# Optimization experiments

Hardware: AMD Instinct MI355X
Metric: run time of the kernel (lower is better)

The kernel has to match this reference:

```python
import jax, jax.numpy as jnp
import numpy as np

DIM = 256
NUM_HEADS = 8
HEAD_DIM = DIM // NUM_HEADS          # 32
KEY_DIM = int(HEAD_DIM * 0.5)        # 16
SCALE = KEY_DIM ** (-0.5)
QKV_OUT = DIM + 2 * KEY_DIM * NUM_HEADS  # 512
BN_EPS = 1e-3


def _bn(x, gamma, beta, mean, var):
    # inference-mode BatchNorm2d over channel axis 1 of NCHW
    inv = gamma / jnp.sqrt(var + BN_EPS)
    return x * inv[None, :, None, None] + (beta - mean * inv)[None, :, None, None]


def _conv1x1(x, w):
    # w: (O, C, 1, 1)
    return jnp.einsum('bchw,oc->bohw', x, w[:, :, 0, 0])


def _dwconv3x3(x, w):
    # depthwise 3x3, SAME padding; w: (C, 1, 3, 3)
    return jax.lax.conv_general_dilated(
        x, w, window_strides=(1, 1), padding='SAME',
        feature_group_count=x.shape[1],
        dimension_numbers=('NCHW', 'OIHW', 'NCHW'))


def setup_inputs() -> dict:
    key = jax.random.key(0)
    ks = jax.random.split(key, 16)
    B, C, H, W = 16, DIM, 32, 32
    inp = {
        'x': jax.random.normal(ks[0], (B, C, H, W), jnp.float32),
        'qkv_w': jax.random.normal(ks[1], (QKV_OUT, DIM, 1, 1), jnp.float32) * (1.0 / np.sqrt(DIM)),
        'qkv_gamma': jnp.ones((QKV_OUT,), jnp.float32),
        'qkv_beta': jnp.zeros((QKV_OUT,), jnp.float32),
        'qkv_mean': jax.random.normal(ks[2], (QKV_OUT,), jnp.float32) * 0.1,
        'qkv_var': jax.random.uniform(ks[3], (QKV_OUT,), jnp.float32, 0.5, 1.5),
        'pe_w': jax.random.normal(ks[4], (DIM, 1, 3, 3), jnp.float32) * (1.0 / 3.0),
        'pe_gamma': jnp.ones((DIM,), jnp.float32),
        'pe_beta': jnp.zeros((DIM,), jnp.float32),
        'pe_mean': jax.random.normal(ks[5], (DIM,), jnp.float32) * 0.1,
        'pe_var': jax.random.uniform(ks[6], (DIM,), jnp.float32, 0.5, 1.5),
        'proj_w': jax.random.normal(ks[7], (DIM, DIM, 1, 1), jnp.float32) * (1.0 / np.sqrt(DIM)),
        'proj_gamma': jnp.ones((DIM,), jnp.float32),
        'proj_beta': jnp.zeros((DIM,), jnp.float32),
        'proj_mean': jax.random.normal(ks[8], (DIM,), jnp.float32) * 0.1,
        'proj_var': jax.random.uniform(ks[9], (DIM,), jnp.float32, 0.5, 1.5),
    }
    return inp


def reference(x, qkv_w, qkv_gamma, qkv_beta, qkv_mean, qkv_var,
              pe_w, pe_gamma, pe_beta, pe_mean, pe_var,
              proj_w, proj_gamma, proj_beta, proj_mean, proj_var):
    B, C, H, W = x.shape
    N = H * W
    # qkv: 1x1 conv + BN (act=False)
    qkv = _bn(_conv1x1(x, qkv_w), qkv_gamma, qkv_beta, qkv_mean, qkv_var)
    qkv = qkv.reshape(B, NUM_HEADS, 2 * KEY_DIM + HEAD_DIM, N)
    q = qkv[:, :, :KEY_DIM]                          # (B, h, kd, N)
    k = qkv[:, :, KEY_DIM:2 * KEY_DIM]               # (B, h, kd, N)
    v = qkv[:, :, 2 * KEY_DIM:]                      # (B, h, hd, N)
    # attn = (q^T @ k) * scale, softmax over last dim
    attn = jnp.einsum('bhdn,bhdm->bhnm', q, k) * SCALE   # (B, h, N, N)
    attn = jax.nn.softmax(attn, axis=-1)
    # v @ attn^T
    v_attn = jnp.einsum('bhdn,bhmn->bhdm', v, attn)      # (B, h, hd, N)
    v_attn = v_attn.reshape(B, C, H, W)
    v_reshaped = v.reshape(B, C, H, W)
    pos_enc = _bn(_dwconv3x3(v_reshaped, pe_w), pe_gamma, pe_beta, pe_mean, pe_var)
    out = v_attn + pos_enc
    out = _bn(_conv1x1(out, proj_w), proj_gamma, proj_beta, proj_mean, proj_var)
    return out
```

## Files before the change

### kernel.cpp

```cpp
#include <hip/hip_runtime.h>

#define B_ 16
#define C_ 256
#define N_ 1024
#define NH 8
#define HD 32
#define KD 16
#define QKV_OUT_ 512
#define BN_EPS 1e-3f
#define SCALE2_ (0.25f * 1.44269504088896f)

typedef __attribute__((ext_vector_type(8))) short short8;
typedef __attribute__((ext_vector_type(16))) float float16;

__device__ inline unsigned short f2bf(float f) {
  unsigned int u = __float_as_uint(f);
  return (unsigned short)((u + 0x7FFF + ((u >> 16) & 1)) >> 16);
}
__device__ inline float bf2f(unsigned short s) {
  return __uint_as_float(((unsigned int)s) << 16);
}
__device__ inline float16 zero16() {
  float16 z;
  #pragma unroll
  for (int i = 0; i < 16; ++i) z[i] = 0.f;
  return z;
}
__device__ inline unsigned int pack_bf16_trunc(float a, float b) {
  return __builtin_amdgcn_perm(__float_as_uint(b), __float_as_uint(a), 0x07060302u);
}
__device__ inline unsigned int pack_bf16_rne(float a, float b) {
  return (unsigned int)f2bf(a) | ((unsigned int)f2bf(b) << 16);
}
__device__ inline float fast_exp2(float x) {
#if __has_builtin(__builtin_amdgcn_exp2f)
  return __builtin_amdgcn_exp2f(x);
#else
  return exp2f(x);
#endif
}
__device__ inline void pl32(unsigned int& a, unsigned int& b) {
#if __has_builtin(__builtin_amdgcn_permlane32_swap)
  typedef __attribute__((ext_vector_type(2))) int int2v;
  int2v r = __builtin_amdgcn_permlane32_swap((int)a, (int)b, false, false);
  a = (unsigned int)r[0];
  b = (unsigned int)r[1];
#else
  unsigned int ea = (unsigned int)__shfl_xor((int)a, 32, 64);
  unsigned int eb = (unsigned int)__shfl_xor((int)b, 32, 64);
  bool hi = (threadIdx.x & 32) != 0;
  unsigned int an = hi ? eb : a;
  unsigned int bn = hi ? b : ea;
  a = an; b = bn;
#endif
}
__device__ inline short8 lds_frag(const unsigned short* p) {
  union { uint2 u[2]; short8 s; } r;
  r.u[0] = *(const uint2*)p;
  r.u[1] = *(const uint2*)(p + 4);
  return r.s;
}
__device__ inline void lds_store16(unsigned short* p, uint4 v) {
  *(uint2*)p = make_uint2(v.x, v.y);
  *(uint2*)(p + 4) = make_uint2(v.z, v.w);
}

__global__ __launch_bounds__(256) void fold_weights(
    const float* __restrict__ qkv_w, const float* __restrict__ qg,
    const float* __restrict__ qb, const float* __restrict__ qm,
    const float* __restrict__ qv,
    const float* __restrict__ proj_w, const float* __restrict__ pg,
    const float* __restrict__ pb, const float* __restrict__ pm,
    const float* __restrict__ pv,
    unsigned short* __restrict__ wq, float* __restrict__ biasq,
    unsigned short* __restrict__ wp, float* __restrict__ biasp)
{
  const int o = blockIdx.x, c = threadIdx.x;
  if (o < QKV_OUT_) {
    float s = ((o & 63) < 16) ? SCALE2_ : 1.f;
    float inv = qg[o] * rsqrtf(qv[o] + BN_EPS) * s;
    wq[o * C_ + c] = f2bf(qkv_w[o * C_ + c] * inv);
    if (c == 0) biasq[o] = qb[o] * s - qm[o] * inv;
  } else {
    int oo = o - QKV_OUT_;
    float inv = pg[oo] * rsqrtf(pv[oo] + BN_EPS);
    wp[oo * C_ + c] = f2bf(proj_w[oo * C_ + c] * inv);
    if (c == 0) biasp[oo] = pb[oo] - pm[oo] * inv;
  }
}

__global__ __launch_bounds__(256) void gemm_qkv(
    const float* __restrict__ x, const unsigned short* __restrict__ wq,
    const float* __restrict__ bias,
    unsigned short* __restrict__ qkT, unsigned short* __restrict__ vbuf)
{
  constexpr int STR = 44;
  __shared__ __align__(8) unsigned short wa[2][128 * STR];
  __shared__ __align__(8) unsigned short xb[2][128 * STR];
  const int tid = threadIdx.x;
  const int wave = tid >> 6, lane = tid & 63, l31 = lane & 31, lh = lane >> 5;
  const int wm = wave & 1, wn = wave >> 1;
  const int b = blockIdx.x >> 3, nloc = (blockIdx.x & 7) * 128;
  const int o0 = blockIdx.y * 128;

  const int r0 = tid >> 2, oc0 = (tid & 3) * 8;
  const int r1 = r0 + 64;
  const int tok = tid & 127, chalf = (tid >> 7) * 16;
  const float* xbase = x + (size_t)b * C_ * N_ + nloc + tok;

  uint4 ga0, ga1;
  float nb[16];

  auto loadk = [&](int kc) {
    ga0 = *(const uint4*)(wq + (size_t)(o0 + r0) * C_ + kc * 32 + oc0);
    ga1 = *(const uint4*)(wq + (size_t)(o0 + r1) * C_ + kc * 32 + oc0);
    #pragma unroll
    for (int j = 0; j < 16; ++j)
      nb[j] = xbase[(size_t)(kc * 32 + chalf + j) * N_];
  };
  auto storek = [&](int bufi) {
    lds_store16(&wa[bufi][r0 * STR + oc0], ga0);
    lds_store16(&wa[bufi][r1 * STR + oc0], ga1);
    unsigned int pk[8];
    #pragma unroll
    for (int q = 0; q < 8; ++q) pk[q] = pack_bf16_rne(nb[2 * q], nb[2 * q + 1]);
    lds_store16(&xb[bufi][tok * STR + chalf], make_uint4(pk[0], pk[1], pk[2], pk[3]));
    lds_store16(&xb[bufi][tok * STR + chalf + 8], make_uint4(pk[4], pk[5], pk[6], pk[7]));
  };

  float16 acc[2][2];
  #pragma unroll
  for (int i = 0; i < 2; ++i)
    #pragma unroll
    for (int j = 0; j < 2; ++j) acc[i][j] = zero16();

  loadk(0);
  storek(0);
  __syncthreads();

  for (int kc = 0; kc < 8; ++kc) {
    const int buf = kc & 1;
    if (kc < 7) loadk(kc + 1);

    #pragma unroll
    for (int ks = 0; ks < 2; ++ks) {
      const int ko = ks * 16 + lh * 8;
      short8 a0 = lds_frag(&wa[buf][(wm * 64 + l31) * STR + ko]);
      short8 a1 = lds_frag(&wa[buf][(wm * 64 + 32 + l31) * STR + ko]);
      short8 b0 = lds_frag(&xb[buf][(wn * 64 + l31) * STR + ko]);
      short8 b1 = lds_frag(&xb[buf][(wn * 64 + 32 + l31) * STR + ko]);
      acc[0][0] = __builtin_amdgcn_mfma_f32_32x32x16_bf16(a0, b0, acc[0][0], 0, 0, 0);
      acc[0][1] = __builtin_amdgcn_mfma_f32_32x32x16_bf16(a0, b1, acc[0][1], 0, 0, 0);
      acc[1][0] = __builtin_amdgcn_mfma_f32_32x32x16_bf16(a1, b0, acc[1][0], 0, 0, 0);
      acc[1][1] = __builtin_amdgcn_mfma_f32_32x32x16_bf16(a1, b1, acc[1][1], 0, 0, 0);
    }

    if (kc < 7) storek(buf ^ 1);
    __syncthreads();
  }

  const int hh = (o0 >> 6) + wm;
  #pragma unroll
  for (int bn = 0; bn < 2; ++bn) {
    int n = nloc + wn * 64 + bn * 32 + l31;
    unsigned short* row = qkT + (((size_t)b * NH + hh) * N_ + n) * 32;
    #pragma unroll
    for (int qd = 0; qd < 4; ++qd) {
      int cc0 = 8 * qd + 4 * lh;
      ushort4 rv;
      rv.x = f2bf(acc[0][bn][4 * qd + 0] + bias[hh * 64 + cc0 + 0]);
      rv.y = f2bf(acc[0][bn][4 * qd + 1] + bias[hh * 64 + cc0 + 1]);
      rv.z = f2bf(acc[0][bn][4 * qd + 2] + bias[hh * 64 + cc0 + 2]);
      rv.w = f2bf(acc[0][bn][4 * qd + 3] + bias[hh * 64 + cc0 + 3]);
      *(ushort4*)(row + cc0) = rv;
    }
  }
  #pragma unroll
  for (int r = 0; r < 16; ++r) {
    int d = (r & 3) + 8 * (r >> 2) + 4 * lh;
    float bo = bias[hh * 64 + 32 + d];
    unsigned short* vrow =
        vbuf + ((size_t)b * C_ + hh * 32 + d) * N_ + nloc + wn * 64 + l31;
    #pragma unroll
    for (int bn = 0; bn < 2; ++bn)
      vrow[bn * 32] = f2bf(acc[1][bn][r] + bo);
  }
}

__global__ __launch_bounds__(256) void gemm_proj(
    const unsigned short* __restrict__ inT, const unsigned short* __restrict__ wp,
    const float* __restrict__ bias, float* __restrict__ outf)
{
  constexpr int STR = 44;
  __shared__ __align__(8) unsigned short wa[2][64 * STR];
  __shared__ __align__(8) unsigned short xb[2][128 * STR];
  const int tid = threadIdx.x;
  const int wave = tid >> 6, lane = tid & 63, l31 = lane & 31, lh = lane >> 5;
  const int wm = wave & 1, wn = wave >> 1;
  const int n0g = blockIdx.x * 128;
  const int o0 = blockIdx.y * 64;
  const int b = n0g >> 10, nloc = n0g & 1023;

  const int ar = tid >> 2, aseg = (tid & 3) * 8;

  float16 acc[2];
  acc[0] = zero16(); acc[1] = zero16();

  uint4 ga, gb0, gb1;
  auto loadk = [&](int kc) {
    ga  = *(const uint4*)(wp + (size_t)(o0 + ar) * C_ + kc * 32 + aseg);
    gb0 = *(const uint4*)(inT + (size_t)(n0g + ar) * C_ + kc * 32 + aseg);
    gb1 = *(const uint4*)(inT + (size_t)(n0g + ar + 64) * C_ + kc * 32 + aseg);
  };
  auto storek = [&](int bufi) {
    lds_store16(&wa[bufi][ar * STR + aseg], ga);
    lds_store16(&xb[bufi][ar * STR + aseg], gb0);
    lds_store16(&xb[bufi][(ar + 64) * STR + aseg], gb1);
  };

  loadk(0);
  storek(0);
  __syncthreads();

  for (int kc = 0; kc < 8; ++kc) {
    const int buf = kc & 1;
    if (kc < 7) loadk(kc + 1);

    #pragma unroll
    for (int ks = 0; ks < 2; ++ks) {
      const int ko = ks * 16 + lh * 8;
      short8 a0 = lds_frag(&wa[buf][(wm * 32 + l31) * STR + ko]);
      short8 b0 = lds_frag(&xb[buf][(wn * 64 + l31) * STR + ko]);
      short8 b1 = lds_frag(&xb[buf][(wn * 64 + 32 + l31) * STR + ko]);
      acc[0] = __builtin_amdgcn_mfma_f32_32x32x16_bf16(a0, b0, acc[0], 0, 0, 0);
      acc[1] = __builtin_amdgcn_mfma_f32_32x32x16_bf16(a0, b1, acc[1], 0, 0, 0);
    }

    if (kc < 7) storek(buf ^ 1);
    __syncthreads();
  }

  #pragma unroll
  for (int r = 0; r < 16; ++r) {
    int o = o0 + wm * 32 + (r & 3) + 8 * (r >> 2) + 4 * lh;
    float bo = bias[o];
    float* orow = outf + ((size_t)b * C_ + o) * N_ + nloc + wn * 64 + l31;
    #pragma unroll
    for (int bn = 0; bn < 2; ++bn)
      orow[bn * 32] = acc[bn][r] + bo;
  }
}

__global__ __launch_bounds__(256) void attn_mfma(
    const unsigned short* __restrict__ qkT, const unsigned short* __restrict__ vbuf,
    const float* __restrict__ pw, const float* __restrict__ peg,
    const float* __restrict__ peb, const float* __restrict__ pem,
    const float* __restrict__ pev, unsigned short* __restrict__ vattnT)
{
  __shared__ __align__(16) unsigned short k_lds[2][128 * 28];
  __shared__ __align__(16) unsigned short v_lds[2][32 * 140];

  const int tid = threadIdx.x;
  const int wave = tid >> 6, lane = tid & 63;
  const int l31 = lane & 31, lh = lane >> 5;
  const int b = blockIdx.x >> 3, h = blockIdx.x & 7;
  const int qbase = blockIdx.y * 128 + wave * 32;

  const unsigned short* qkb = qkT + ((size_t)b * NH + h) * N_ * 32;
  const unsigned short* vhead = vbuf + ((size_t)b * C_ + h * HD) * N_;

  const int skey = tid >> 1, shalf = tid & 1;
  const int svd = tid >> 3, svseg = tid & 7;

  short8 qf = *(const short8*)(qkb + (size_t)(qbase + l31) * 32 + lh * 8);

  uint4 gk, gv0, gv1;
  auto loadc = [&](int kc) {
    gk  = *(const uint4*)(qkb + (size_t)(kc + skey) * 32 + 16 + shalf * 8);
    gv0 = *(const uint4*)(vhead + (size_t)svd * N_ + kc + svseg * 16);
    gv1 = *(const uint4*)(vhead + (size_t)svd * N_ + kc + svseg * 16 + 8);
  };
  auto storec = [&](int bufi) {
    lds_store16(&k_lds[bufi][skey * 28 + shalf * 8], gk);
    lds_store16(&v_lds[bufi][svd * 140 + svseg * 16], gv0);
    lds_store16(&v_lds[bufi][svd * 140 + svseg * 16 + 8], gv1);
  };

  loadc(0);
  storec(0);
  __syncthreads();

  float16 oaccE = zero16(), oaccO = zero16();
  float ls[4] = {0.f, 0.f, 0.f, 0.f};

  for (int c = 0; c < 8; ++c) {
    const int buf = c & 1;
    if (c < 7) loadc((c + 1) * 128);

    #pragma unroll
    for (int t = 0; t < 4; ++t) {
      const int key0 = t * 32;
      short8 kf = lds_frag(&k_lds[buf][(key0 + l31) * 28 + lh * 8]);
      float16 st = __builtin_amdgcn_mfma_f32_32x32x16_bf16(kf, qf, zero16(), 0, 0, 0);

      unsigned int u[8];
      #pragma unroll
      for (int q = 0; q < 8; ++q) {
        float pe = fast_exp2(st[2 * q]);
        float po = fast_exp2(st[2 * q + 1]);
        ls[q & 3] += pe + po;
        u[q] = pack_bf16_trunc(pe, po);
      }

      #pragma unroll
      for (int f = 0; f < 2; ++f) {
        short8 vf = lds_frag(&v_lds[buf][l31 * 140 + key0 + f * 16 + lh * 8]);
        const int q0 = f * 4;
        unsigned int a0 = u[q0], a2 = u[q0 + 2]; pl32(a0, a2);
        unsigned int a1 = u[q0 + 1], a3 = u[q0 + 3]; pl32(a1, a3);
        union { unsigned int w[4]; short8 s; } bf;
        bf.w[0] = a0; bf.w[1] = a1; bf.w[2] = a2; bf.w[3] = a3;
        if (f == 0)
          oaccE = __builtin_amdgcn_mfma_f32_32x32x16_bf16(vf, bf.s, oaccE, 0, 0, 0);
        else
          oaccO = __builtin_amdgcn_mfma_f32_32x32x16_bf16(vf, bf.s, oaccO, 0, 0, 0);
      }
    }

    if (c < 7) storec(buf ^ 1);
    __syncthreads();
  }

  const int R0 = blockIdx.y * 4;
  unsigned short* ptb = &v_lds[0][0] + 8;
  float* w12 = (float*)&k_lds[0][0];
  unsigned short* pout = (unsigned short*)((char*)&k_lds[0][0] + 32 * 12 * 4);

  if (tid == 0) lds_store16(&v_lds[0][0], make_uint4(0, 0, 0, 0));
  if (tid < 192) {
    const int d = tid / 6, ry = tid - d * 6;
    unsigned short* dst = ptb + d * 240 + ry * 40;
    const uint4 z = make_uint4(0, 0, 0, 0);
    lds_store16(dst + 32, z);
    const int yy = R0 - 1 + ry;
    if (yy >= 0 && yy < 32) {
      const unsigned short* src = vhead + (size_t)d * N_ + yy * 32;
      lds_store16(dst,      *(const uint4*)(src));
      lds_store16(dst + 8,  *(const uint4*)(src + 8));
      lds_store16(dst + 16, *(const uint4*)(src + 16));
      lds_store16(dst + 24, *(const uint4*)(src + 24));
    } else {
      lds_store16(dst, z); lds_store16(dst + 8, z);
      lds_store16(dst + 16, z); lds_store16(dst + 24, z);
    }
  }
  if (tid < 32) {
    const int cg = h * HD + tid;
    const float iv = peg[cg] * rsqrtf(pev[cg] + BN_EPS);
    float* wr = w12 + tid * 12;
    #pragma unroll
    for (int k = 0; k < 9; ++k) wr[k] = pw[cg * 9 + k] * iv;
    wr[9] = peb[cg] - pem[cg] * iv;
    wr[10] = 0.f; wr[11] = 0.f;
  }
  __syncthreads();

  {
    const int d = tid >> 3, row = (tid >> 1) & 3, x0 = (tid & 1) * 16;
    const float* wr = w12 + d * 12;
    float wv[10];
    #pragma unroll
    for (int k = 0; k < 10; ++k) wv[k] = wr[k];
    float acc[16];
    #pragma unroll
    for (int j = 0; j < 16; ++j) acc[j] = wv[9];
    #pragma unroll
    for (int dy = 0; dy < 3; ++dy) {
      const unsigned short* base = ptb + d * 240 + (row + dy) * 40 + x0;
      float tv[18];
      tv[0] = bf2f(base[-1]);
      short8 s0 = lds_frag(base);
      short8 s1 = lds_frag(base + 8);
      #pragma unroll
      for (int j = 0; j < 8; ++j) {
        tv[1 + j] = bf2f((unsigned short)s0[j]);
        tv[9 + j] = bf2f((unsigned short)s1[j]);
      }
      tv[17] = bf2f(base[16]);
      const float w0 = wv[dy * 3], w1 = wv[dy * 3 + 1], w2 = wv[dy * 3 + 2];
      #pragma unroll
      for (int j = 0; j < 16; ++j)
        acc[j] += w0 * tv[j] + w1 * tv[j + 1] + w2 * tv[j + 2];
    }
    unsigned short* po = pout + d * 128 + row * 32 + x0;
    unsigned int pk[8];
    #pragma unroll
    for (int q = 0; q < 8; ++q) pk[q] = pack_bf16_rne(acc[2 * q], acc[2 * q + 1]);
    lds_store16(po,     make_uint4(pk[0], pk[1], pk[2], pk[3]));
    lds_store16(po + 8, make_uint4(pk[4], pk[5], pk[6], pk[7]));
  }
  __syncthreads();

  float lsum = (ls[0] + ls[1]) + (ls[2] + ls[3]);
  lsum += __shfl_xor(lsum, 32, 64);
  const float linv = 1.f / lsum;

  const int token = qbase + l31;
  float val[16];
  #pragma unroll
  for (int r = 0; r < 16; ++r) {
    int d = (r & 3) + 8 * (r >> 2) + 4 * lh;
    val[r] = (oaccE[r] + oaccO[r]) * linv +
             bf2f(pout[d * 128 + wave * 32 + l31]);
  }
  unsigned int u[8];
  #pragma unroll
  for (int m = 0; m < 8; ++m) u[m] = pack_bf16_rne(val[2 * m], val[2 * m + 1]);
  pl32(u[0], u[4]); pl32(u[1], u[5]); pl32(u[2], u[6]); pl32(u[3], u[7]);
  unsigned short* row = vattnT + ((size_t)b * N_ + token) * C_ + h * HD + lh * 16;
  *(uint4*)(row)     = make_uint4(u[0], u[1], u[4], u[5]);
  *(uint4*)(row + 8) = make_uint4(u[2], u[3], u[6], u[7]);
}

extern "C" void kernel_launch(void* const* d_in, const int* in_sizes, int n_in,
                              void* d_out, int out_size, void* d_ws, size_t ws_size,
                              hipStream_t stream) {
  const float* x          = (const float*)d_in[0];
  const float* qkv_w      = (const float*)d_in[1];
  const float* qkv_gamma  = (const float*)d_in[2];
  const float* qkv_beta   = (const float*)d_in[3];
  const float* qkv_mean   = (const float*)d_in[4];
  const float* qkv_var    = (const float*)d_in[5];
  const float* pe_w       = (const float*)d_in[6];
  const float* pe_gamma   = (const float*)d_in[7];
  const float* pe_beta    = (const float*)d_in[8];
  const float* pe_mean    = (const float*)d_in[9];
  const float* pe_var     = (const float*)d_in[10];
  const float* proj_w     = (const float*)d_in[11];
  const float* proj_gamma = (const float*)d_in[12];
  const float* proj_beta  = (const float*)d_in[13];
  const float* proj_mean  = (const float*)d_in[14];
  const float* proj_var   = (const float*)d_in[15];
  float* out = (float*)d_out;

  char* ws = (char*)d_ws;
  unsigned short* qkT = (unsigned short*)ws;
  ws += (size_t)B_ * NH * N_ * 32 * sizeof(unsigned short);
  unsigned short* vbuf = (unsigned short*)ws;
  ws += (size_t)B_ * C_ * N_ * sizeof(unsigned short);
  unsigned short* vattnT = (unsigned short*)ws;
  ws += (size_t)B_ * N_ * C_ * sizeof(unsigned short);
  unsigned short* wq = (unsigned short*)ws;
  ws += (size_t)QKV_OUT_ * C_ * sizeof(unsigned short);
  unsigned short* wp = (unsigned short*)ws;
  ws += (size_t)C_ * C_ * sizeof(unsigned short);
  float* biasq = (float*)ws; ws += QKV_OUT_ * sizeof(float);
  float* biasp = (float*)ws;

  fold_weights<<<dim3(QKV_OUT_ + C_), 256, 0, stream>>>(
      qkv_w, qkv_gamma, qkv_beta, qkv_mean, qkv_var,
      proj_w, proj_gamma, proj_beta, proj_mean, proj_var,
      wq, biasq, wp, biasp);

  gemm_qkv<<<dim3(128, 4), 256, 0, stream>>>(x, wq, biasq, qkT, vbuf);

  attn_mfma<<<dim3(128, 8), 256, 0, stream>>>(
      qkT, vbuf, pe_w, pe_gamma, pe_beta, pe_mean, pe_var, vattnT);

  gemm_proj<<<dim3(128, 4), 256, 0, stream>>>(vattnT, wp, biasp, out);
}
```

Baseline: 153.0 us.

## Process two query tiles per wave in attention to reuse K/V fragments

```diff
diff --git a/kernel.cpp b/kernel.cpp
--- a/kernel.cpp
+++ b/kernel.cpp
@@ -251,20 +251,21 @@
   }
 }
 
-__global__ __launch_bounds__(256) void attn_mfma(
+__global__ __launch_bounds__(256, 2) void attn_mfma(
     const unsigned short* __restrict__ qkT, const unsigned short* __restrict__ vbuf,
     const float* __restrict__ pw, const float* __restrict__ peg,
     const float* __restrict__ peb, const float* __restrict__ pem,
     const float* __restrict__ pev, unsigned short* __restrict__ vattnT)
 {
-  __shared__ __align__(16) unsigned short k_lds[2][128 * 28];
-  __shared__ __align__(16) unsigned short v_lds[2][32 * 140];
+  __shared__ __align__(16) unsigned short smem[21792];
+  unsigned short* kl = smem;
+  unsigned short* vl = smem + 7168;
 
   const int tid = threadIdx.x;
   const int wave = tid >> 6, lane = tid & 63;
   const int l31 = lane & 31, lh = lane >> 5;
   const int b = blockIdx.x >> 3, h = blockIdx.x & 7;
-  const int qbase = blockIdx.y * 128 + wave * 32;
+  const int qbase = blockIdx.y * 256 + wave * 64;
 
   const unsigned short* qkb = qkT + ((size_t)b * NH + h) * N_ * 32;
   const unsigned short* vhead = vbuf + ((size_t)b * C_ + h * HD) * N_;
@@ -272,7 +273,8 @@
   const int skey = tid >> 1, shalf = tid & 1;
   const int svd = tid >> 3, svseg = tid & 7;
 
-  short8 qf = *(const short8*)(qkb + (size_t)(qbase + l31) * 32 + lh * 8);
+  short8 qfE = *(const short8*)(qkb + (size_t)(qbase + l31) * 32 + lh * 8);
+  short8 qfF = *(const short8*)(qkb + (size_t)(qbase + 32 + l31) * 32 + lh * 8);
 
   uint4 gk, gv0, gv1;
   auto loadc = [&](int kc) {
@@ -281,17 +283,18 @@
     gv1 = *(const uint4*)(vhead + (size_t)svd * N_ + kc + svseg * 16 + 8);
   };
   auto storec = [&](int bufi) {
-    lds_store16(&k_lds[bufi][skey * 28 + shalf * 8], gk);
-    lds_store16(&v_lds[bufi][svd * 140 + svseg * 16], gv0);
-    lds_store16(&v_lds[bufi][svd * 140 + svseg * 16 + 8], gv1);
+    lds_store16(&kl[bufi * 3584 + skey * 28 + shalf * 8], gk);
+    lds_store16(&vl[bufi * 4480 + svd * 140 + svseg * 16], gv0);
+    lds_store16(&vl[bufi * 4480 + svd * 140 + svseg * 16 + 8], gv1);
   };
 
   loadc(0);
   storec(0);
   __syncthreads();
 
-  float16 oaccE = zero16(), oaccO = zero16();
-  float ls[4] = {0.f, 0.f, 0.f, 0.f};
+  float16 o0E = zero16(), o0O = zero16(), o1E = zero16(), o1O = zero16();
+  float lsE[4] = {0.f, 0.f, 0.f, 0.f};
+  float lsF[4] = {0.f, 0.f, 0.f, 0.f};
 
   for (int c = 0; c < 8; ++c) {
     const int buf = c & 1;
@@ -300,58 +303,86 @@
     #pragma unroll
     for (int t = 0; t < 4; ++t) {
       const int key0 = t * 32;
-      short8 kf = lds_frag(&k_lds[buf][(key0 + l31) * 28 + lh * 8]);
-      float16 st = __builtin_amdgcn_mfma_f32_32x32x16_bf16(kf, qf, zero16(), 0, 0, 0);
-
-      unsigned int u[8];
+      short8 kf  = lds_frag(&kl[buf * 3584 + (key0 + l31) * 28 + lh * 8]);
+      short8 vf0 = lds_frag(&vl[buf * 4480 + l31 * 140 + key0 + lh * 8]);
+      short8 vf1 = lds_frag(&vl[buf * 4480 + l31 * 140 + key0 + 16 + lh * 8]);
+
+      __builtin_amdgcn_s_setprio(1);
+      float16 stE = __builtin_amdgcn_mfma_f32_32x32x16_bf16(kf, qfE, zero16(), 0, 0, 0);
+      float16 stF = __builtin_amdgcn_mfma_f32_32x32x16_bf16(kf, qfF, zero16(), 0, 0, 0);
+      __builtin_amdgcn_s_setprio(0);
+
+      unsigned int uE[8], uF[8];
       #pragma unroll
       for (int q = 0; q < 8; ++q) {
-        float pe = fast_exp2(st[2 * q]);
-        float po = fast_exp2(st[2 * q + 1]);
-        ls[q & 3] += pe + po;
-        u[q] = pack_bf16_trunc(pe, po);
+        float pe = fast_exp2(stE[2 * q]);
+        float po = fast_exp2(stE[2 * q + 1]);
+        lsE[q & 3] += pe + po;
+        uE[q] = pack_bf16_trunc(pe, po);
       }
-
       #pragma unroll
-      for (int f = 0; f < 2; ++f) {
-        short8 vf = lds_frag(&v_lds[buf][l31 * 140 + key0 + f * 16 + lh * 8]);
-        const int q0 = f * 4;
-        unsigned int a0 = u[q0], a2 = u[q0 + 2]; pl32(a0, a2);
-        unsigned int a1 = u[q0 + 1], a3 = u[q0 + 3]; pl32(a1, a3);
-        union { unsigned int w[4]; short8 s; } bf;
-        bf.w[0] = a0; bf.w[1] = a1; bf.w[2] = a2; bf.w[3] = a3;
-        if (f == 0)
-          oaccE = __builtin_amdgcn_mfma_f32_32x32x16_bf16(vf, bf.s, oaccE, 0, 0, 0);
-        else
-          oaccO = __builtin_amdgcn_mfma_f32_32x32x16_bf16(vf, bf.s, oaccO, 0, 0, 0);
+      for (int q = 0; q < 8; ++q) {
+        float pe = fast_exp2(stF[2 * q]);
+        float po = fast_exp2(stF[2 * q + 1]);
+        lsF[q & 3] += pe + po;
+        uF[q] = pack_bf16_trunc(pe, po);
       }
+
+      union { unsigned int w[4]; short8 s; } bE0, bE1, bF0, bF1;
+      {
+        unsigned int a0 = uE[0], a2 = uE[2]; pl32(a0, a2);
+        unsigned int a1 = uE[1], a3 = uE[3]; pl32(a1, a3);
+        bE0.w[0] = a0; bE0.w[1] = a1; bE0.w[2] = a2; bE0.w[3] = a3;
+        unsigned int c0 = uE[4], c2 = uE[6]; pl32(c0, c2);
+        unsigned int c1 = uE[5], c3 = uE[7]; pl32(c1, c3);
+        bE1.w[0] = c0; bE1.w[1] = c1; bE1.w[2] = c2; bE1.w[3] = c3;
+      }
+      {
+        unsigned int a0 = uF[0], a2 = uF[2]; pl32(a0, a2);
+        unsigned int a1 = uF[1], a3 = uF[3]; pl32(a1, a3);
+        bF0.w[0] = a0; bF0.w[1] = a1; bF0.w[2] = a2; bF0.w[3] = a3;
+        unsigned int c0 = uF[4], c2 = uF[6]; pl32(c0, c2);
+        unsigned int c1 = uF[5], c3 = uF[7]; pl32(c1, c3);
+        bF1.w[0] = c0; bF1.w[1] = c1; bF1.w[2] = c2; bF1.w[3] = c3;
+      }
+
+      __builtin_amdgcn_s_setprio(1);
+      o0E = __builtin_amdgcn_mfma_f32_32x32x16_bf16(vf0, bE0.s, o0E, 0, 0, 0);
+      o1E = __builtin_amdgcn_mfma_f32_32x32x16_bf16(vf0, bF0.s, o1E, 0, 0, 0);
+      o0O = __builtin_amdgcn_mfma_f32_32x32x16_bf16(vf1, bE1.s, o0O, 0, 0, 0);
+      o1O = __builtin_amdgcn_mfma_f32_32x32x16_bf16(vf1, bF1.s, o1O, 0, 0, 0);
+      __builtin_amdgcn_s_setprio(0);
     }
 
     if (c < 7) storec(buf ^ 1);
     __syncthreads();
   }
 
-  const int R0 = blockIdx.y * 4;
-  unsigned short* ptb = &v_lds[0][0] + 8;
-  float* w12 = (float*)&k_lds[0][0];
-  unsigned short* pout = (unsigned short*)((char*)&k_lds[0][0] + 32 * 12 * 4);
-
-  if (tid == 0) lds_store16(&v_lds[0][0], make_uint4(0, 0, 0, 0));
-  if (tid < 192) {
-    const int d = tid / 6, ry = tid - d * 6;
-    unsigned short* dst = ptb + d * 240 + ry * 40;
-    const uint4 z = make_uint4(0, 0, 0, 0);
-    lds_store16(dst + 32, z);
-    const int yy = R0 - 1 + ry;
-    if (yy >= 0 && yy < 32) {
-      const unsigned short* src = vhead + (size_t)d * N_ + yy * 32;
-      lds_store16(dst,      *(const uint4*)(src));
-      lds_store16(dst + 8,  *(const uint4*)(src + 8));
-      lds_store16(dst + 16, *(const uint4*)(src + 16));
-      lds_store16(dst + 24, *(const uint4*)(src + 24));
-    } else {
-      lds_store16(dst, z); lds_store16(dst + 8, z);
-      lds_store16(dst + 16, z); lds_store16(dst + 24, z);
+  const int R0 = blockIdx.y * 8;
+  float* w12 = (float*)smem;
+  unsigned short* ptb = smem + 776;
+  unsigned short* pout = smem + 13576;
+
+  if (tid == 0) lds_store16(&smem[768], make_uint4(0, 0, 0, 0));
+  #pragma unroll
+  for (int it = 0; it < 2; ++it) {
+    const int i = tid + it * 256;
+    if (i < 320) {
+      const int d = i / 10, ry = i - d * 10;
+      unsigned short* dst = ptb + d * 400 + ry * 40;
+      const uint4 z = make_uint4(0, 0, 0, 0);
+      lds_store16(dst + 32, z);
+      const int yy = R0 - 1 + ry;
+      if (yy >= 0 && yy < 32) {
+        const unsigned short* src = vhead + (size_t)d * N_ + yy * 32;
+        lds_store16(dst,      *(const uint4*)(src));
+        lds_store16(dst + 8,  *(const uint4*)(src + 8));
+        lds_store16(dst + 16, *(const uint4*)(src + 16));
+        lds_store16(dst + 24, *(const uint4*)(src + 24));
+      } else {
+        lds_store16(dst, z); lds_store16(dst + 8, z);
+        lds_store16(dst + 16, z); lds_store16(dst + 24, z);
+      }
     }
   }
   if (tid < 32) {
@@ -365,8 +396,10 @@
   }
   __syncthreads();
 
-  {
-    const int d = tid >> 3, row = (tid >> 1) & 3, x0 = (tid & 1) * 16;
+  #pragma unroll
+  for (int it = 0; it < 2; ++it) {
+    const int item = tid + it * 256;
+    const int d = item >> 4, row = (item >> 1) & 7, x0 = (item & 1) * 16;
     const float* wr = w12 + d * 12;
     float wv[10];
     #pragma unroll
@@ -376,7 +409,7 @@
     for (int j = 0; j < 16; ++j) acc[j] = wv[9];
     #pragma unroll
     for (int dy = 0; dy < 3; ++dy) {
-      const unsigned short* base = ptb + d * 240 + (row + dy) * 40 + x0;
+      const unsigned short* base = ptb + d * 400 + (row + dy) * 40 + x0;
       float tv[18];
       tv[0] = bf2f(base[-1]);
       short8 s0 = lds_frag(base);
@@ -392,7 +425,7 @@
       for (int j = 0; j < 16; ++j)
         acc[j] += w0 * tv[j] + w1 * tv[j + 1] + w2 * tv[j + 2];
     }
-    unsigned short* po = pout + d * 128 + row * 32 + x0;
+    unsigned short* po = pout + d * 256 + row * 32 + x0;
     unsigned int pk[8];
     #pragma unroll
     for (int q = 0; q < 8; ++q) pk[q] = pack_bf16_rne(acc[2 * q], acc[2 * q + 1]);
@@ -401,25 +434,32 @@
   }
   __syncthreads();
 
-  float lsum = (ls[0] + ls[1]) + (ls[2] + ls[3]);
-  lsum += __shfl_xor(lsum, 32, 64);
-  const float linv = 1.f / lsum;
-
-  const int token = qbase + l31;
-  float val[16];
-  #pragma unroll
-  for (int r = 0; r < 16; ++r) {
-    int d = (r & 3) + 8 * (r >> 2) + 4 * lh;
-    val[r] = (oaccE[r] + oaccO[r]) * linv +
-             bf2f(pout[d * 128 + wave * 32 + l31]);
-  }
-  unsigned int u[8];
-  #pragma unroll
-  for (int m = 0; m < 8; ++m) u[m] = pack_bf16_rne(val[2 * m], val[2 * m + 1]);
-  pl32(u[0], u[4]); pl32(u[1], u[5]); pl32(u[2], u[6]); pl32(u[3], u[7]);
-  unsigned short* row = vattnT + ((size_t)b * N_ + token) * C_ + h * HD + lh * 16;
-  *(uint4*)(row)     = make_uint4(u[0], u[1], u[4], u[5]);
-  *(uint4*)(row + 8) = make_uint4(u[2], u[3], u[6], u[7]);
+  float lsumE = (lsE[0] + lsE[1]) + (lsE[2] + lsE[3]);
+  lsumE += __shfl_xor(lsumE, 32, 64);
+  const float linvE = 1.f / lsumE;
+  float lsumF = (lsF[0] + lsF[1]) + (lsF[2] + lsF[3]);
+  lsumF += __shfl_xor(lsumF, 32, 64);
+  const float linvF = 1.f / lsumF;
+
+  auto emit = [&](const float16& aE, const float16& aO, float linv, int g) {
+    const int token = qbase + g * 32 + l31;
+    const int yl = wave * 2 + g;
+    float val[16];
+    #pragma unroll
+    for (int r = 0; r < 16; ++r) {
+      int d = (r & 3) + 8 * (r >> 2) + 4 * lh;
+      val[r] = (aE[r] + aO[r]) * linv + bf2f(pout[d * 256 + yl * 32 + l31]);
+    }
+    unsigned int u[8];
+    #pragma unroll
+    for (int m = 0; m < 8; ++m) u[m] = pack_bf16_rne(val[2 * m], val[2 * m + 1]);
+    pl32(u[0], u[4]); pl32(u[1], u[5]); pl32(u[2], u[6]); pl32(u[3], u[7]);
+    unsigned short* row = vattnT + ((size_t)b * N_ + token) * C_ + h * HD + lh * 16;
+    *(uint4*)(row)     = make_uint4(u[0], u[1], u[4], u[5]);
+    *(uint4*)(row + 8) = make_uint4(u[2], u[3], u[6], u[7]);
+  };
+  emit(o0E, o0O, linvE, 0);
+  emit(o1E, o1O, linvF, 1);
 }
 
 extern "C" void kernel_launch(void* const* d_in, const int* in_sizes, int n_in,
@@ -464,7 +504,7 @@
 
   gemm_qkv<<<dim3(128, 4), 256, 0, stream>>>(x, wq, biasq, qkT, vbuf);
 
-  attn_mfma<<<dim3(128, 8), 256, 0, stream>>>(
+  attn_mfma<<<dim3(128, 4), 256, 0, stream>>>(
       qkT, vbuf, pe_w, pe_gamma, pe_beta, pe_mean, pe_var, vattnT);
 
   gemm_proj<<<dim3(128, 4), 256, 0, stream>>>(vattnT, wp, biasp, out);
```

Result: faster. 146.6 us (-4.2%).
